# Kernel optimization log

Measured on AMD Instinct MI355X. Metric: run time of the kernel, lower is better.

The kernel has to match this reference:

```python
import jax, jax.numpy as jnp
import numpy as np
import math

ALPHA = math.exp(-0.001 * 1000.0)  # exp(-dt * tau_filter_inv)
T, B, D_IN, D_OUT = 2048, 32, 512, 512


def setup_inputs() -> dict:
    key = jax.random.key(0)
    k1, k2, k3 = jax.random.split(key, 3)
    bound = 1.0 / math.sqrt(D_IN)  # torch Linear default init range
    return {
        "input_tensor": jax.random.normal(k1, (T, B, D_IN), dtype=jnp.float32),
        "weight": jax.random.uniform(k2, (D_OUT, D_IN), minval=-bound, maxval=bound, dtype=jnp.float32),
        "bias": jax.random.uniform(k3, (D_OUT,), minval=-bound, maxval=bound, dtype=jnp.float32),
    }


def reference(input_tensor, weight, bias):
    # y[t] = W x[t] + b   -> [T, B, D_OUT]
    y = jnp.einsum("tbi,oi->tbo", input_tensor, weight) + bias
    alpha = jnp.asarray(ALPHA, dtype=y.dtype)

    # out[0] = y[0]; out[t] = alpha * out[t-1] + y[t]
    def step(carry, yt):
        out = alpha * carry + yt
        return out, out

    _, rest = jax.lax.scan(step, y[0], y[1:])
    return jnp.concatenate([y[:1], rest], axis=0)
```

## Files before the change

### kernel.cpp

```cpp
#include <hip/hip_runtime.h>
#include <stdint.h>

#define T_DIM 2048
#define B_DIM 32
#define DIN   512
#define DOUT  512
#define M_DIM (T_DIM * B_DIM)
#define COLS  (B_DIM * DIN)
#define COLS4 (COLS / 4)

#define ALPHA_F 0.36787944117144233f
#define INV_1MA 1.5819767068693265f

#define CHUNKS   64
#define CHUNK_T  32
#define HALO     8

#define FCHUNKS  32
#define FCHUNK_T 64
#define FHALO    16

typedef float  floatx4 __attribute__((ext_vector_type(4)));
typedef __bf16 bf16x8  __attribute__((ext_vector_type(8)));

__device__ __forceinline__ uint32_t pk2(float a, float b) {
  uint32_t ua = __float_as_uint(a); ua += 0x7fffu + ((ua >> 16) & 1u);
  uint32_t ub = __float_as_uint(b); ub += 0x7fffu + ((ub >> 16) & 1u);
  return (ua >> 16) | (ub & 0xffff0000u);
}

__device__ __forceinline__ void gload_lds16(const void* g, void* lds) {
  __builtin_amdgcn_global_load_lds(
      (const __attribute__((address_space(1))) void*)g,
      (__attribute__((address_space(3))) void*)lds,
      16, 0, 0);
}

__device__ __forceinline__ void fma4(float4& c, const float4& v) {
  c.x = fmaf(ALPHA_F, c.x, v.x);
  c.y = fmaf(ALPHA_F, c.y, v.y);
  c.z = fmaf(ALPHA_F, c.z, v.z);
  c.w = fmaf(ALPHA_F, c.w, v.w);
}

__global__ void wconv_kernel(const float* __restrict__ W,
                             uint16_t* __restrict__ WB)
{
  const int t = blockIdx.x * 256 + threadIdx.x;
  const float4* W4 = (const float4*)W;
#pragma unroll
  for (int j = 0; j < 8; ++j) {
    const int b4 = t * 16 + j * 2;
    float4 w0 = W4[b4], w1 = W4[b4 + 1];
    uint4 p;
    p.x = pk2(w0.x, w0.y); p.y = pk2(w0.z, w0.w);
    p.z = pk2(w1.x, w1.y); p.w = pk2(w1.z, w1.w);
    *(uint4*)&WB[t * 64 + j * 8] = p;
  }
}

template<bool HAS_HALO>
__device__ __forceinline__ void filter_chunk(const float4* __restrict__ X4,
                                             uint16_t* __restrict__ XF,
                                             size_t base)
{
  constexpr int NSTEP = HAS_HALO ? (CHUNK_T + HALO) : CHUNK_T;
  const size_t b0 = HAS_HALO ? (base - (size_t)HALO * COLS4) : base;

  float4 ring[4];
  float4 carry = {0.0f, 0.0f, 0.0f, 0.0f};

#pragma unroll
  for (int j = 0; j < 4; ++j) ring[j] = X4[b0 + (size_t)j * COLS4];

#pragma unroll
  for (int s = 0; s < NSTEP; ++s) {
    float4 v = ring[s & 3];
    if (s + 4 < NSTEP) ring[s & 3] = X4[b0 + (size_t)(s + 4) * COLS4];
    fma4(carry, v);
    const int t = HAS_HALO ? (s - HALO) : s;
    if (t >= 0) {
      uint2 p;
      p.x = pk2(carry.x, carry.y);
      p.y = pk2(carry.z, carry.w);
      *(uint2*)&XF[(base + (size_t)t * COLS4) * 4] = p;
    }
  }
}

__global__ void filter_x_kernel(const float* __restrict__ X,
                                uint16_t* __restrict__ XF)
{
  const int col4 = blockIdx.x * 256 + threadIdx.x;
  const int c = blockIdx.y;
  const float4* X4 = (const float4*)X;
  const size_t base = (size_t)c * CHUNK_T * COLS4 + col4;

  if (c > 0) filter_chunk<true>(X4, XF, base);
  else       filter_chunk<false>(X4, XF, base);
}

__launch_bounds__(256, 4)
__global__ void gemm_bf16_kernel(const uint16_t* __restrict__ XF,
                                 const uint16_t* __restrict__ WB,
                                 const float* __restrict__ bias,
                                 float* __restrict__ Y)
{
  __shared__ __align__(16) uint16_t As[128 * 64];
  __shared__ __align__(16) uint16_t Bs[128 * 64];

  const int bid = blockIdx.x;
  const int lg = (bid & 7) * 256 + (bid >> 3);
  const int n0 = (lg & 3) * 128;
  const int m0 = (lg >> 2) * 128;

  const int tid  = threadIdx.x;
  const int lane = tid & 63;
  const int w    = tid >> 6;
  const int r    = lane & 15;
  const int q    = lane >> 4;
  const int wm   = w >> 1;
  const int wn   = w & 1;

  const int srow_base = w * 32 + (lane >> 3);
  const int schunk    = lane & 7;

  floatx4 acc[4][4];
#pragma unroll
  for (int i = 0; i < 4; ++i)
#pragma unroll
    for (int j = 0; j < 4; ++j) {
      floatx4 z = {0.0f, 0.0f, 0.0f, 0.0f};
      acc[i][j] = z;
    }

  for (int kt = 0; kt < DIN / 64; ++kt) {
    const int k0 = kt * 64;
#pragma unroll
    for (int i = 0; i < 4; ++i) {
      const int row = srow_base + i * 8;
      const int sc = schunk ^ (row & 7);
      gload_lds16(XF + (size_t)(m0 + row) * DIN + k0 + sc * 8,
                  &As[(w * 32 + i * 8) * 64]);
      gload_lds16(WB + (size_t)(n0 + row) * DIN + k0 + sc * 8,
                  &Bs[(w * 32 + i * 8) * 64]);
    }
    __syncthreads();

#pragma unroll
    for (int kk = 0; kk < 2; ++kk) {
      bf16x8 af[4], bfr[4];
#pragma unroll
      for (int mi = 0; mi < 4; ++mi) {
        const int row = wm * 64 + mi * 16 + r;
        const int cch = (kk * 4 + q) ^ (row & 7);
        af[mi] = *(const bf16x8*)&As[row * 64 + (cch << 3)];
      }
#pragma unroll
      for (int ni = 0; ni < 4; ++ni) {
        const int row = wn * 64 + ni * 16 + r;
        const int cch = (kk * 4 + q) ^ (row & 7);
        bfr[ni] = *(const bf16x8*)&Bs[row * 64 + (cch << 3)];
      }
#pragma unroll
      for (int mi = 0; mi < 4; ++mi)
#pragma unroll
        for (int ni = 0; ni < 4; ++ni)
          acc[mi][ni] = __builtin_amdgcn_mfma_f32_16x16x32_bf16(
              af[mi], bfr[ni], acc[mi][ni], 0, 0, 0);
    }
    __syncthreads();
  }

#pragma unroll
  for (int mi = 0; mi < 4; ++mi) {
    const int rowb = m0 + wm * 64 + mi * 16;
    const int t = rowb >> 5;
    const float s = (1.0f - __expf(-(float)(t + 1))) * INV_1MA;
#pragma unroll
    for (int ni = 0; ni < 4; ++ni) {
      const int col = n0 + wn * 64 + ni * 16 + r;
      const float sb = s * bias[col];
#pragma unroll
      for (int j = 0; j < 4; ++j)
        Y[(size_t)(rowb + q * 4 + j) * DOUT + col] = acc[mi][ni][j] + sb;
    }
  }
}

__launch_bounds__(256, 2)
__global__ void gemm_bias_kernel(const float* __restrict__ X,
                                 const float* __restrict__ W,
                                 const float* __restrict__ bias,
                                 float* __restrict__ Y,
                                 float* __restrict__ halo,
                                 int halo_on)
{
  __shared__ __align__(16) uint16_t As[128 * 64];
  __shared__ __align__(16) uint16_t Bsh[128 * 64];

  const int tid  = threadIdx.x;
  const int lane = tid & 63;
  const int wave = tid >> 6;
  const int wm   = wave >> 1;
  const int wn   = wave & 1;
  const int r    = lane & 15;
  const int q    = lane >> 4;

  const int m0 = blockIdx.y * 128;
  const int n0 = blockIdx.x * 128;

  floatx4 acc[4][4];
#pragma unroll
  for (int i = 0; i < 4; ++i)
#pragma unroll
    for (int j = 0; j < 4; ++j) {
      floatx4 z = {0.0f, 0.0f, 0.0f, 0.0f};
      acc[i][j] = z;
    }

  for (int kt = 0; kt < DIN / 64; ++kt) {
    const int k0 = kt * 64;
#pragma unroll
    for (int j = 0; j < 4; ++j) {
      const int cid = tid + j * 256;
      const int row = cid >> 3;
      const int c   = cid & 7;
      const int slot = (c ^ (row & 7)) << 3;

      const float* ga = &X[(size_t)(m0 + row) * DIN + k0 + c * 8];
      float4 a0 = *(const float4*)ga;
      float4 a1 = *(const float4*)(ga + 4);
      uint4 pa;
      pa.x = pk2(a0.x, a0.y); pa.y = pk2(a0.z, a0.w);
      pa.z = pk2(a1.x, a1.y); pa.w = pk2(a1.z, a1.w);
      *(uint4*)&As[row * 64 + slot] = pa;

      const float* gb = &W[(size_t)(n0 + row) * DIN + k0 + c * 8];
      float4 b0 = *(const float4*)gb;
      float4 b1 = *(const float4*)(gb + 4);
      uint4 pb;
      pb.x = pk2(b0.x, b0.y); pb.y = pk2(b0.z, b0.w);
      pb.z = pk2(b1.x, b1.y); pb.w = pk2(b1.z, b1.w);
      *(uint4*)&Bsh[row * 64 + slot] = pb;
    }
    __syncthreads();

#pragma unroll
    for (int kk = 0; kk < 2; ++kk) {
      bf16x8 af[4], bfr[4];
#pragma unroll
      for (int mi = 0; mi < 4; ++mi) {
        const int row = wm * 64 + mi * 16 + r;
        const int c   = (kk * 4 + q) ^ (row & 7);
        af[mi] = *(const bf16x8*)&As[row * 64 + (c << 3)];
      }
#pragma unroll
      for (int ni = 0; ni < 4; ++ni) {
        const int row = wn * 64 + ni * 16 + r;
        const int c   = (kk * 4 + q) ^ (row & 7);
        bfr[ni] = *(const bf16x8*)&Bsh[row * 64 + (c << 3)];
      }
#pragma unroll
      for (int mi = 0; mi < 4; ++mi)
#pragma unroll
        for (int ni = 0; ni < 4; ++ni)
          acc[mi][ni] = __builtin_amdgcn_mfma_f32_16x16x32_bf16(
              af[mi], bfr[ni], acc[mi][ni], 0, 0, 0);
    }
    __syncthreads();
  }

#pragma unroll
  for (int ni = 0; ni < 4; ++ni) {
    const int col = n0 + wn * 64 + ni * 16 + r;
    const float bv = bias[col];
#pragma unroll
    for (int mi = 0; mi < 4; ++mi) {
      const int rowm = m0 + wm * 64 + mi * 16 + q * 4;
      const int t = rowm >> 5;
      const int b = rowm & 31;
      const int tloc = t & (FCHUNK_T - 1);
      const bool hw = halo_on && (tloc >= FCHUNK_T - FHALO) && (t < T_DIM - FCHUNK_T);
      const size_t hbase = hw
          ? ((size_t)(((t >> 6) + 1) * FHALO + (tloc - (FCHUNK_T - FHALO))) * COLS)
          : 0;
#pragma unroll
      for (int j = 0; j < 4; ++j) {
        const float v = acc[mi][ni][j] + bv;
        Y[(size_t)(rowm + j) * DOUT + col] = v;
        if (hw) halo[hbase + (size_t)(b + j) * DOUT + col] = v;
      }
    }
  }
}

__global__ void scan_kernel(float* __restrict__ Y,
                            const float* __restrict__ halo,
                            int chunk_len)
{
  const int col4 = blockIdx.x * blockDim.x + threadIdx.x;
  const int c = blockIdx.y;

  float4* Y4 = (float4*)Y;
  const float4* H4 = (const float4*)halo;

  float4 carry = {0.0f, 0.0f, 0.0f, 0.0f};
  if (c > 0) {
#pragma unroll
    for (int h = 0; h < FHALO; ++h) {
      float4 v = H4[(size_t)(c * FHALO + h) * COLS4 + col4];
      fma4(carry, v);
    }
  }

  size_t idx = (size_t)c * chunk_len * COLS4 + col4;
  float4 ynext = Y4[idx];
  for (int t = 0; t < chunk_len; ++t) {
    float4 y = ynext;
    if (t + 1 < chunk_len) ynext = Y4[idx + COLS4];
    fma4(carry, y);
    Y4[idx] = carry;
    idx += COLS4;
  }
}

extern "C" void kernel_launch(void* const* d_in, const int* in_sizes, int n_in,
                              void* d_out, int out_size, void* d_ws, size_t ws_size,
                              hipStream_t stream)
{
  const float* X    = (const float*)d_in[0];
  const float* W    = (const float*)d_in[1];
  const float* bias = (const float*)d_in[2];
  float* Y = (float*)d_out;

  const size_t need_new = (size_t)M_DIM * DIN * 2 + (size_t)DOUT * DIN * 2;

  if (ws_size >= need_new) {
    uint16_t* XF = (uint16_t*)d_ws;
    uint16_t* WB = XF + (size_t)M_DIM * DIN;

    wconv_kernel<<<16, 256, 0, stream>>>(W, WB);
    dim3 gf(16, CHUNKS);
    filter_x_kernel<<<gf, 256, 0, stream>>>(X, XF);
    gemm_bf16_kernel<<<2048, 256, 0, stream>>>(XF, WB, bias, Y);
  } else {
    float* halo = (float*)d_ws;
    const size_t halo_need = (size_t)FCHUNKS * FHALO * COLS * sizeof(float);
    const int halo_on = (ws_size >= halo_need) ? 1 : 0;

    dim3 g1(DOUT / 128, M_DIM / 128);
    gemm_bias_kernel<<<g1, 256, 0, stream>>>(X, W, bias, Y, halo, halo_on);

    const int n_chunks = halo_on ? FCHUNKS : 1;
    dim3 g2(COLS4 / 256, n_chunks);
    scan_kernel<<<g2, 256, 0, stream>>>(Y, halo, T_DIM / n_chunks);
  }
}
```

Baseline: 106.2 us.

## Stage filter input tiles in LDS via async loads and split scan into segments

The time-filter kernel no longer has each thread walk 40 timesteps of one column straight from global memory. Each block now loads a 40-row by 64-float4 tile into LDS with global_load_lds, and four waves each run a short 16-step recurrence (8 halo plus 8 outputs) over their own segment. The grid grows from 1024 to 4096 blocks. This is meant to raise memory-level parallelism and shorten the serial dependency chain per thread, at the cost of LDS use, a block barrier and twice the filter arithmetic per output.

```diff
diff --git a/kernel.cpp b/kernel.cpp
--- a/kernel.cpp
+++ b/kernel.cpp
@@ -12,9 +12,10 @@
 #define ALPHA_F 0.36787944117144233f
 #define INV_1MA 1.5819767068693265f
 
-#define CHUNKS   64
-#define CHUNK_T  32
-#define HALO     8
+#define FT_T    32
+#define FT_HALO 8
+#define FT_ROWS (FT_T + FT_HALO)
+#define FT_C4   64
 
 #define FCHUNKS  32
 #define FCHUNK_T 64
@@ -59,45 +60,57 @@
   }
 }
 
-template<bool HAS_HALO>
-__device__ __forceinline__ void filter_chunk(const float4* __restrict__ X4,
-                                             uint16_t* __restrict__ XF,
-                                             size_t base)
-{
-  constexpr int NSTEP = HAS_HALO ? (CHUNK_T + HALO) : CHUNK_T;
-  const size_t b0 = HAS_HALO ? (base - (size_t)HALO * COLS4) : base;
-
-  float4 ring[4];
+__global__ void filter_x_kernel(const float* __restrict__ X,
+                                uint16_t* __restrict__ XF)
+{
+  __shared__ __align__(16) float lds[FT_ROWS * FT_C4 * 4];
+
+  const int ct = blockIdx.x;
+  const int tt = blockIdx.y;
+  const int tid  = threadIdx.x;
+  const int lane = tid & 63;
+  const int w    = tid >> 6;
+  const int t0   = tt * FT_T;
+  const size_t gc4 = (size_t)ct * FT_C4;
+
+  float4* L4 = (float4*)lds;
+
+  if (tt == 0) {
+    const float4 z = {0.0f, 0.0f, 0.0f, 0.0f};
+#pragma unroll
+    for (int i = 0; i < 2; ++i)
+      L4[tid + i * 256] = z;
+#pragma unroll
+    for (int i = 0; i < 8; ++i) {
+      const int row = 8 + w + i * 4;
+      gload_lds16(X + ((size_t)(t0 + row - 8) * COLS4 + gc4 + lane) * 4,
+                  &L4[row * FT_C4]);
+    }
+  } else {
+#pragma unroll
+    for (int i = 0; i < 10; ++i) {
+      const int row = w + i * 4;
+      gload_lds16(X + ((size_t)(t0 - 8 + row) * COLS4 + gc4 + lane) * 4,
+                  &L4[row * FT_C4]);
+    }
+  }
+  __syncthreads();
+
+  const int seg = w;
   float4 carry = {0.0f, 0.0f, 0.0f, 0.0f};
-
-#pragma unroll
-  for (int j = 0; j < 4; ++j) ring[j] = X4[b0 + (size_t)j * COLS4];
-
-#pragma unroll
-  for (int s = 0; s < NSTEP; ++s) {
-    float4 v = ring[s & 3];
-    if (s + 4 < NSTEP) ring[s & 3] = X4[b0 + (size_t)(s + 4) * COLS4];
+#pragma unroll
+  for (int j = 0; j < 16; ++j) {
+    const int r = seg * 8 + j;
+    float4 v = L4[r * FT_C4 + lane];
     fma4(carry, v);
-    const int t = HAS_HALO ? (s - HALO) : s;
-    if (t >= 0) {
+    if (j >= 8) {
+      const int o = seg * 8 + j - 8;
       uint2 p;
       p.x = pk2(carry.x, carry.y);
       p.y = pk2(carry.z, carry.w);
-      *(uint2*)&XF[(base + (size_t)t * COLS4) * 4] = p;
-    }
-  }
-}
-
-__global__ void filter_x_kernel(const float* __restrict__ X,
-                                uint16_t* __restrict__ XF)
-{
-  const int col4 = blockIdx.x * 256 + threadIdx.x;
-  const int c = blockIdx.y;
-  const float4* X4 = (const float4*)X;
-  const size_t base = (size_t)c * CHUNK_T * COLS4 + col4;
-
-  if (c > 0) filter_chunk<true>(X4, XF, base);
-  else       filter_chunk<false>(X4, XF, base);
+      *(uint2*)&XF[((size_t)(t0 + o) * COLS4 + gc4 + lane) * 4] = p;
+    }
+  }
 }
 
 __launch_bounds__(256, 4)
@@ -341,7 +354,7 @@
     uint16_t* WB = XF + (size_t)M_DIM * DIN;
 
     wconv_kernel<<<16, 256, 0, stream>>>(W, WB);
-    dim3 gf(16, CHUNKS);
+    dim3 gf(COLS4 / FT_C4, T_DIM / FT_T);
     filter_x_kernel<<<gf, 256, 0, stream>>>(X, XF);
     gemm_bf16_kernel<<<2048, 256, 0, stream>>>(XF, WB, bias, Y);
   } else {
```

New measurement: 91.38 us. -14.0%, faster.
